# Optimization experiments

Hardware: AMD Instinct MI355X
Metric: run time of the kernel (lower is better)

The kernel has to match this reference:

```python
import jax, jax.numpy as jnp
import numpy as np

K = 3
PAD = 1
STRIDE = 1


def _conv2d(x, w, b, stride, pad):
    y = jax.lax.conv_general_dilated(
        x, w, window_strides=(stride, stride), padding=[(pad, pad), (pad, pad)],
        dimension_numbers=("NCHW", "OIHW", "NCHW"))
    return y + b[None, :, None, None]


def _deform_conv(x, offsets, w_def, stride, pad):
    B, C, H, W = x.shape
    Cout = w_def.shape[0]
    Ho, Wo = offsets.shape[2], offsets.shape[3]
    K2 = K * K
    # torchvision layout: offsets[:, 2*k] = dy, offsets[:, 2*k+1] = dx for tap k = i*K + j
    off = offsets.reshape(B, K2, 2, Ho, Wo)
    dy, dx = off[:, :, 0], off[:, :, 1]  # [B,K2,Ho,Wo]
    k = jnp.arange(K2)
    iy = (k // K).astype(x.dtype)  # kernel tap row
    ix = (k % K).astype(x.dtype)
    hs = (jnp.arange(Ho) * stride - pad).astype(x.dtype)
    ws = (jnp.arange(Wo) * stride - pad).astype(x.dtype)
    py = hs[None, None, :, None] + iy[None, :, None, None] + dy  # [B,K2,Ho,Wo]
    px = ws[None, None, None, :] + ix[None, :, None, None] + dx
    y0 = jnp.floor(py)
    x0 = jnp.floor(px)
    wy = py - y0
    wx = px - x0
    x_flat = x.reshape(B, C, H * W)

    def gather(yi, xi, wgt):
        valid = (yi >= 0) & (yi < H) & (xi >= 0) & (xi < W)
        yic = jnp.clip(yi, 0, H - 1).astype(jnp.int32)
        xic = jnp.clip(xi, 0, W - 1).astype(jnp.int32)
        idx = (yic * W + xic).reshape(B, -1)  # [B, K2*Ho*Wo]
        g = jax.vmap(lambda xf, i: xf[:, i])(x_flat, idx)  # [B,C,K2*Ho*Wo]
        return g * (wgt * valid).reshape(B, 1, -1)

    val = gather(y0, x0, (1 - wy) * (1 - wx))
    val = val + gather(y0, x0 + 1, (1 - wy) * wx)
    val = val + gather(y0 + 1, x0, wy * (1 - wx))
    val = val + gather(y0 + 1, x0 + 1, wy * wx)
    val = val.reshape(B, C, K2, Ho, Wo)  # bilinear-sampled im2col
    return jnp.einsum('bckhw,ock->bohw', val, w_def.reshape(Cout, C, K2))


def setup_inputs() -> dict:
    key = jax.random.key(0)
    k1, k2, k3, k4 = jax.random.split(key, 4)
    B, C, H, W, Cout = 8, 128, 64, 64, 128
    x = jax.random.normal(k1, (B, C, H, W), dtype=jnp.float32)
    w_off = jax.random.normal(k2, (2 * K * K, C, K, K), dtype=jnp.float32) * 0.01
    b_off = jax.random.normal(k3, (2 * K * K,), dtype=jnp.float32) * 0.01
    w_def = jax.random.normal(k4, (Cout, C, K, K), dtype=jnp.float32) * (1.0 / np.sqrt(C * K * K))
    return {"x": x, "w_off": w_off, "b_off": b_off, "w_def": w_def}


def reference(x, w_off, b_off, w_def):
    offsets = _conv2d(x, w_off, b_off, STRIDE, PAD)
    return _deform_conv(x, offsets, w_def, STRIDE, PAD)
```

## Files before the change

### kernel.cpp

```cpp
#include <hip/hip_runtime.h>
#include <hip/hip_bf16.h>

#define B_    8
#define C_    128
#define H_    64
#define W_    64
#define COUT_ 128
#define K2_   9
#define JOFF_ 18
#define HW_   (H_*W_)
#define CK_   (C_*K2_)

typedef short  short8 __attribute__((ext_vector_type(8)));
typedef float  f32x4  __attribute__((ext_vector_type(4)));

__device__ __forceinline__ ushort f2bf(float f) {
    __hip_bfloat16 h = __float2bfloat16(f);
    return *reinterpret_cast<ushort*>(&h);
}
__device__ __forceinline__ float bf2f(ushort u) {
    return __uint_as_float(((uint)u) << 16);
}
__device__ __forceinline__ uint bfround(float f) {
    uint u = __float_as_uint(f);
    return u + 0x7FFFu + ((u >> 16) & 1u);
}
__device__ __forceinline__ uint bfpack(float v0, float v1) {
    return __builtin_amdgcn_perm(bfround(v1), bfround(v0), 0x07060302u);
}

__global__ __launch_bounds__(512) void nhwc_kernel(
    const float* __restrict__ x, ushort* __restrict__ xt)
{
    __shared__ float tile[64][65];
    const int blk = blockIdx.x;
    const int ht = blk & 63;
    const int ct = (blk >> 6) & 1;
    const int b  = blk >> 7;
    const int t  = threadIdx.x;
    const int tx = t & 63, ty = t >> 6;

    const float* xs = x + ((size_t)(b * C_ + ct * 64) << 12) + (ht << 6);
#pragma unroll
    for (int i = 0; i < 8; ++i) {
        int c = i * 8 + ty;
        tile[c][tx] = xs[((size_t)c << 12) + tx];
    }
    __syncthreads();

    const int r  = t >> 3;
    const int co = (t & 7) * 8;
    short8 pack;
#pragma unroll
    for (int j = 0; j < 8; ++j) pack[j] = (short)f2bf(tile[co + j][r]);
    *reinterpret_cast<short8*>(
        xt + ((((size_t)b << 12) + (ht << 6) + r) << 7) + ct * 64 + co) = pack;
}

__global__ __launch_bounds__(256) void transpose_w_kernel(
    const float* __restrict__ w_def, const float* __restrict__ w_off,
    ushort* __restrict__ wt, ushort* __restrict__ wt_off)
{
    int t = blockIdx.x * 256 + threadIdx.x;
    if (t < K2_ * COUT_ * C_) {
        int c = t & 127;
        int o = (t >> 7) & 127;
        int k = t >> 14;
        float v = w_def[((size_t)o * C_ + c) * K2_ + k];
        wt[((size_t)k * COUT_ + o) * C_ + c] = f2bf(v);
    } else {
        int i = t - K2_ * COUT_ * C_;
        if (i < K2_ * 32 * C_) {
            int c = i & 127;
            int j = (i >> 7) & 31;
            int k = i >> 12;
            float v = (j < JOFF_) ? w_off[((size_t)j * C_ + c) * K2_ + k] : 0.f;
            wt_off[(((size_t)k * 32) + j) * C_ + c] = f2bf(v);
        }
    }
}

__global__ __launch_bounds__(512, 4) void deform_mfma_kernel(
    const ushort* __restrict__ xt, const ushort* __restrict__ wt,
    const ushort* __restrict__ wt_off, const float* __restrict__ b_off,
    float* __restrict__ out)
{
    __shared__ __align__(16) ushort smem[3 * 66 * C_];
    __shared__ float s_off[JOFF_][64];

    typedef ushort sB_t[2][64][C_];
    typedef ushort pro_t[3][66][C_];
    sB_t&  sB  = *reinterpret_cast<sB_t*>(smem);
    pro_t& pro = *reinterpret_cast<pro_t*>(smem);

    const int bid  = blockIdx.x;
    const int nbid = ((bid & 7) << 6) + (bid >> 3);
    const int s0   = nbid << 6;
    const int b    = s0 >> 12;
    const int hw0  = s0 & (HW_ - 1);
    const int ho   = hw0 >> 6;

    const int t    = threadIdx.x;
    const int wid  = t >> 6, lane = t & 63;
    const int arow = lane & 15;
    const int akk  = (lane >> 4) << 3;
    const int gp   = t >> 3;
    const int gq   = t & 7;
    const int swzp = (gp & 15) << 3;
    const ushort* xtb = xt + ((size_t)b << 19);

    if (t < 384) {
        int rr  = t >> 7, sub = t & 127;
        int q   = (sub & 64) ? 65 : 0;
        reinterpret_cast<uint*>(&pro[rr][q][0])[sub & 63] = 0u;
    }
#pragma unroll
    for (int it = 0; it < 6; ++it) {
        int i   = t + it * 512;
        int rr  = i >> 10;
        int rem = i & 1023;
        int pos = rem >> 4;
        int ch  = rem & 15;
        int yr  = ho - 1 + rr;
        short8 val = {};
        if (yr >= 0 && yr < H_)
            val = *reinterpret_cast<const short8*>(
                xtb + (((size_t)((yr << 6) + pos)) << 7) + ch * 8);
        int q = pos + 1;
        *reinterpret_cast<short8*>(
            &pro[rr][q][(ch * 8) ^ ((q & 7) << 3)]) = val;
    }
    __syncthreads();

    {
        const int wmO = wid >> 2, wnO = wid & 3;
        const int colq = wnO * 16 + arow;
        f32x4 o0 = {}, o1 = {};
#pragma unroll
        for (int k = 0; k < K2_; ++k) {
            const int ky = k / 3, kx = k % 3;
            const int qr  = colq + kx;
            const int key = (qr & 7) << 3;
            const ushort* ap = wt_off
                + (((size_t)(k * 32 + wmO * 16 + arow)) << 7) + akk;
#pragma unroll
            for (int kc = 0; kc < 4; ++kc) {
                short8 aO = *reinterpret_cast<const short8*>(ap + kc * 32);
                short8 bO = *reinterpret_cast<const short8*>(
                    &pro[ky][qr][(kc * 32 + akk) ^ key]);
                if (kc < 2) o0 = __builtin_amdgcn_mfma_f32_16x16x32_bf16(aO, bO, o0, 0, 0, 0);
                else        o1 = __builtin_amdgcn_mfma_f32_16x16x32_bf16(aO, bO, o1, 0, 0, 0);
            }
        }
        const int sO = wnO * 16 + arow;
#pragma unroll
        for (int r4 = 0; r4 < 4; ++r4) {
            int j = wmO * 16 + ((lane >> 4) << 2) + r4;
            if (j < JOFF_) s_off[j][sO] = o0[r4] + o1[r4] + b_off[j];
        }
    }
    __syncthreads();

    f32x4  acc[4] = {};
    short8 aA[4], aB[4];
    short8 gA[4][2], gB[4][2];
    float  cA[4], cB[4];

    auto load_a = [&](int k, short8 (&dst)[4]) {
        const ushort* wk = wt + (size_t)k * (COUT_ * C_)
                         + (wid * 16 + arow) * C_ + akk;
#pragma unroll
        for (int kc = 0; kc < 4; ++kc)
            dst[kc] = *reinterpret_cast<const short8*>(wk + kc * 32);
    };

    auto gather_load = [&](int k, short8 (&g)[4][2], float (&ca)[4]) {
        float dy = s_off[2*k    ][gp];
        float dx = s_off[2*k + 1][gp];
        float py = (float)(ho - 1 + k/3) + dy;
        float px = (float)(gp - 1 + k%3) + dx;
        float y0f = floorf(py), x0f = floorf(px);
        float wy = py - y0f,    wx = px - x0f;
        int y0 = (int)y0f, x0 = (int)x0f;
        int y1 = y0 + 1,   x1 = x0 + 1;
        float vy0 = (y0 >= 0 && y0 < H_) ? 1.f : 0.f;
        float vy1 = (y1 >= 0 && y1 < H_) ? 1.f : 0.f;
        float vx0 = (x0 >= 0 && x0 < W_) ? 1.f : 0.f;
        float vx1 = (x1 >= 0 && x1 < W_) ? 1.f : 0.f;
        int y0c = min(max(y0, 0), H_-1), y1c = min(max(y1, 0), H_-1);
        int x0c = min(max(x0, 0), W_-1), x1c = min(max(x1, 0), W_-1);
        int bx  = min(max(x0, 0), W_-2);
        float wx0 = (1.f - wx) * vx0, wx1 = wx * vx1;
        float ex0 = (x0c == bx ? wx0 : 0.f) + (x1c == bx ? wx1 : 0.f);
        float ex1 = (x0c == bx ? 0.f : wx0) + (x1c == bx ? 0.f : wx1);
        float r0 = (1.f - wy) * vy0, r1 = wy * vy1;
        ca[0] = r0*ex0; ca[1] = r0*ex1; ca[2] = r1*ex0; ca[3] = r1*ex1;
        const ushort* r00 = xtb + (((y0c << 6) + bx) << 7) + gq * 8;
        const ushort* r10 = xtb + (((y1c << 6) + bx) << 7) + gq * 8;
        g[0][0] = *reinterpret_cast<const short8*>(r00);
        g[0][1] = *reinterpret_cast<const short8*>(r00 + 64);
        g[1][0] = *reinterpret_cast<const short8*>(r00 + 128);
        g[1][1] = *reinterpret_cast<const short8*>(r00 + 192);
        g[2][0] = *reinterpret_cast<const short8*>(r10);
        g[2][1] = *reinterpret_cast<const short8*>(r10 + 64);
        g[3][0] = *reinterpret_cast<const short8*>(r10 + 128);
        g[3][1] = *reinterpret_cast<const short8*>(r10 + 192);
    };

    auto gather_math_store = [&](int buf, const short8 (&g)[4][2],
                                 const float (&ca)[4]) {
#pragma unroll
        for (int j = 0; j < 2; ++j) {
            float v[8];
#pragma unroll
            for (int q = 0; q < 8; ++q) {
                float vv = ca[0] * bf2f((ushort)g[0][j][q]);
                vv = fmaf(ca[1], bf2f((ushort)g[1][j][q]), vv);
                vv = fmaf(ca[2], bf2f((ushort)g[2][j][q]), vv);
                vv = fmaf(ca[3], bf2f((ushort)g[3][j][q]), vv);
                v[q] = vv;
            }
            uint4 pk;
            pk.x = bfpack(v[0], v[1]);
            pk.y = bfpack(v[2], v[3]);
            pk.z = bfpack(v[4], v[5]);
            pk.w = bfpack(v[6], v[7]);
            *reinterpret_cast<uint4*>(
                &sB[buf][gp][(gq * 8 + j * 64) ^ swzp]) = pk;
        }
    };

    load_a(0, aA);
    gather_load(0, gA, cA);
    gather_load(1, gB, cB);
    gather_math_store(0, gA, cA);
    asm volatile("s_waitcnt lgkmcnt(0)" ::: "memory");
    __builtin_amdgcn_s_barrier();

#pragma unroll
    for (int k = 0; k < K2_; ++k) {
        if (k < K2_ - 1) {
            if ((k & 1) == 0) load_a(k + 1, aB);
            else              load_a(k + 1, aA);
        }
        if (k + 2 < K2_) {
            if ((k & 1) == 0) gather_load(k + 2, gA, cA);
            else              gather_load(k + 2, gB, cB);
        }

        {
            const short8 (&a)[4] = ((k & 1) == 0) ? aA : aB;
            const int buf = k & 1;
#pragma unroll
            for (int kc = 0; kc < 4; ++kc) {
#pragma unroll
                for (int ni = 0; ni < 4; ++ni) {
                    int srow = ni*16 + arow;
                    short8 bF = *reinterpret_cast<const short8*>(
                        &sB[buf][srow][(kc*32 + akk) ^ ((srow & 15) << 3)]);
                    acc[ni] = __builtin_amdgcn_mfma_f32_16x16x32_bf16(
                        a[kc], bF, acc[ni], 0, 0, 0);
                }
            }
        }

        if (k < K2_ - 1) {
            if ((k & 1) == 0) gather_math_store((k + 1) & 1, gB, cB);
            else              gather_math_store((k + 1) & 1, gA, cA);
        }

        asm volatile("s_waitcnt lgkmcnt(0)" ::: "memory");
        __builtin_amdgcn_s_barrier();
    }

#pragma unroll
    for (int ni = 0; ni < 4; ++ni) {
#pragma unroll
        for (int r = 0; r < 4; ++r) {
            int o = wid*16 + ((lane >> 4) << 2) + r;
            int s = ni*16 + arow;
            __builtin_nontemporal_store(acc[ni][r],
                &out[(((size_t)(b*COUT_ + o)) << 12) + hw0 + s]);
        }
    }
}

extern "C" void kernel_launch(void* const* d_in, const int* in_sizes, int n_in,
                              void* d_out, int out_size, void* d_ws, size_t ws_size,
                              hipStream_t stream) {
    const float* x     = (const float*)d_in[0];
    const float* w_off = (const float*)d_in[1];
    const float* b_off = (const float*)d_in[2];
    const float* w_def = (const float*)d_in[3];
    float* out  = (float*)d_out;

    char* ws = (char*)d_ws;
    ushort* xtp    = (ushort*)ws;
    ushort* wt     = (ushort*)(ws + 8388608);
    ushort* wt_off = (ushort*)(ws + 8388608 + 294912);

    nhwc_kernel<<<1024, 512, 0, stream>>>(x, xtp);
    {
        int total  = K2_ * COUT_ * C_ + K2_ * 32 * C_;
        transpose_w_kernel<<<(total + 255) / 256, 256, 0, stream>>>(
            w_def, w_off, wt, wt_off);
    }
    deform_mfma_kernel<<<(B_ * HW_) / 64, 512, 0, stream>>>(
        xtp, wt, wt_off, b_off, out);
}
```

Measured before the change: 59.48 us.

## Halve spatial tile to 32 pixels per block and raise occupancy

Each block now covers 32 output pixels instead of 64, which doubles the grid and shrinks the shared-memory prologue and sampling buffers. Launch bounds go from 4 to 6 blocks per CU. The A-weight double buffer becomes a single buffer that is reloaded after the MFMA loop behind a sched_barrier. This lowers register and LDS pressure to gain occupancy, at the cost of reloading the full weight matrix per block and extra halo loads. In the offset conv, waves with wid>=4 now duplicate the work of waves 0-3 and write the same s_off entries.

```diff
diff --git a/kernel.cpp b/kernel.cpp
--- a/kernel.cpp
+++ b/kernel.cpp
@@ -80,60 +80,58 @@
     }
 }
 
-__global__ __launch_bounds__(512, 4) void deform_mfma_kernel(
+__global__ __launch_bounds__(512, 6) void deform_mfma_kernel(
     const ushort* __restrict__ xt, const ushort* __restrict__ wt,
     const ushort* __restrict__ wt_off, const float* __restrict__ b_off,
     float* __restrict__ out)
 {
-    __shared__ __align__(16) ushort smem[3 * 66 * C_];
-    __shared__ float s_off[JOFF_][64];
-
-    typedef ushort sB_t[2][64][C_];
-    typedef ushort pro_t[3][66][C_];
+    __shared__ __align__(16) ushort smem[3 * 34 * C_];
+    __shared__ float s_off[JOFF_][32];
+
+    typedef ushort sB_t[2][32][C_];
+    typedef ushort pro_t[3][34][C_];
     sB_t&  sB  = *reinterpret_cast<sB_t*>(smem);
     pro_t& pro = *reinterpret_cast<pro_t*>(smem);
 
     const int bid  = blockIdx.x;
-    const int nbid = ((bid & 7) << 6) + (bid >> 3);
-    const int s0   = nbid << 6;
+    const int nbid = ((bid & 7) << 7) + (bid >> 3);
+    const int s0   = nbid << 5;
     const int b    = s0 >> 12;
     const int hw0  = s0 & (HW_ - 1);
     const int ho   = hw0 >> 6;
+    const int wo0  = hw0 & 63;
 
     const int t    = threadIdx.x;
     const int wid  = t >> 6, lane = t & 63;
     const int arow = lane & 15;
     const int akk  = (lane >> 4) << 3;
-    const int gp   = t >> 3;
-    const int gq   = t & 7;
+    const int gp   = t >> 4;
+    const int gq   = t & 15;
     const int swzp = (gp & 15) << 3;
     const ushort* xtb = xt + ((size_t)b << 19);
 
-    if (t < 384) {
-        int rr  = t >> 7, sub = t & 127;
-        int q   = (sub & 64) ? 65 : 0;
-        reinterpret_cast<uint*>(&pro[rr][q][0])[sub & 63] = 0u;
-    }
-#pragma unroll
-    for (int it = 0; it < 6; ++it) {
-        int i   = t + it * 512;
-        int rr  = i >> 10;
-        int rem = i & 1023;
-        int pos = rem >> 4;
-        int ch  = rem & 15;
-        int yr  = ho - 1 + rr;
-        short8 val = {};
-        if (yr >= 0 && yr < H_)
-            val = *reinterpret_cast<const short8*>(
-                xtb + (((size_t)((yr << 6) + pos)) << 7) + ch * 8);
-        int q = pos + 1;
-        *reinterpret_cast<short8*>(
-            &pro[rr][q][(ch * 8) ^ ((q & 7) << 3)]) = val;
+#pragma unroll
+    for (int it = 0; it < 4; ++it) {
+        int i = t + it * 512;
+        if (i < 3 * 34 * 16) {
+            int rr  = i / 544;
+            int rem = i - rr * 544;
+            int q   = rem >> 4;
+            int ch  = rem & 15;
+            int yr  = ho - 1 + rr;
+            int sx  = wo0 - 1 + q;
+            short8 val = {};
+            if (yr >= 0 && yr < H_ && sx >= 0 && sx < W_)
+                val = *reinterpret_cast<const short8*>(
+                    xtb + (((size_t)((yr << 6) + sx)) << 7) + ch * 8);
+            *reinterpret_cast<short8*>(
+                &pro[rr][q][(ch * 8) ^ ((q & 7) << 3)]) = val;
+        }
     }
     __syncthreads();
 
     {
-        const int wmO = wid >> 2, wnO = wid & 3;
+        const int wmO = (wid >> 1) & 1, wnO = wid & 1;
         const int colq = wnO * 16 + arow;
         f32x4 o0 = {}, o1 = {};
 #pragma unroll
@@ -161,24 +159,24 @@
     }
     __syncthreads();
 
-    f32x4  acc[4] = {};
-    short8 aA[4], aB[4];
-    short8 gA[4][2], gB[4][2];
+    f32x4  acc[2] = {};
+    short8 aC[4];
+    short8 gA[4], gB[4];
     float  cA[4], cB[4];
 
-    auto load_a = [&](int k, short8 (&dst)[4]) {
+    auto load_a = [&](int k) {
         const ushort* wk = wt + (size_t)k * (COUT_ * C_)
                          + (wid * 16 + arow) * C_ + akk;
 #pragma unroll
         for (int kc = 0; kc < 4; ++kc)
-            dst[kc] = *reinterpret_cast<const short8*>(wk + kc * 32);
+            aC[kc] = *reinterpret_cast<const short8*>(wk + kc * 32);
     };
 
-    auto gather_load = [&](int k, short8 (&g)[4][2], float (&ca)[4]) {
+    auto gather_load = [&](int k, short8 (&g)[4], float (&ca)[4]) {
         float dy = s_off[2*k    ][gp];
         float dx = s_off[2*k + 1][gp];
         float py = (float)(ho - 1 + k/3) + dy;
-        float px = (float)(gp - 1 + k%3) + dx;
+        float px = (float)(wo0 + gp - 1 + k%3) + dx;
         float y0f = floorf(py), x0f = floorf(px);
         float wy = py - y0f,    wx = px - x0f;
         int y0 = (int)y0f, x0 = (int)x0f;
@@ -197,40 +195,32 @@
         ca[0] = r0*ex0; ca[1] = r0*ex1; ca[2] = r1*ex0; ca[3] = r1*ex1;
         const ushort* r00 = xtb + (((y0c << 6) + bx) << 7) + gq * 8;
         const ushort* r10 = xtb + (((y1c << 6) + bx) << 7) + gq * 8;
-        g[0][0] = *reinterpret_cast<const short8*>(r00);
-        g[0][1] = *reinterpret_cast<const short8*>(r00 + 64);
-        g[1][0] = *reinterpret_cast<const short8*>(r00 + 128);
-        g[1][1] = *reinterpret_cast<const short8*>(r00 + 192);
-        g[2][0] = *reinterpret_cast<const short8*>(r10);
-        g[2][1] = *reinterpret_cast<const short8*>(r10 + 64);
-        g[3][0] = *reinterpret_cast<const short8*>(r10 + 128);
-        g[3][1] = *reinterpret_cast<const short8*>(r10 + 192);
+        g[0] = *reinterpret_cast<const short8*>(r00);
+        g[1] = *reinterpret_cast<const short8*>(r00 + 128);
+        g[2] = *reinterpret_cast<const short8*>(r10);
+        g[3] = *reinterpret_cast<const short8*>(r10 + 128);
     };
 
-    auto gather_math_store = [&](int buf, const short8 (&g)[4][2],
+    auto gather_math_store = [&](int buf, const short8 (&g)[4],
                                  const float (&ca)[4]) {
-#pragma unroll
-        for (int j = 0; j < 2; ++j) {
-            float v[8];
-#pragma unroll
-            for (int q = 0; q < 8; ++q) {
-                float vv = ca[0] * bf2f((ushort)g[0][j][q]);
-                vv = fmaf(ca[1], bf2f((ushort)g[1][j][q]), vv);
-                vv = fmaf(ca[2], bf2f((ushort)g[2][j][q]), vv);
-                vv = fmaf(ca[3], bf2f((ushort)g[3][j][q]), vv);
-                v[q] = vv;
-            }
-            uint4 pk;
-            pk.x = bfpack(v[0], v[1]);
-            pk.y = bfpack(v[2], v[3]);
-            pk.z = bfpack(v[4], v[5]);
-            pk.w = bfpack(v[6], v[7]);
-            *reinterpret_cast<uint4*>(
-                &sB[buf][gp][(gq * 8 + j * 64) ^ swzp]) = pk;
-        }
+        float v[8];
+#pragma unroll
+        for (int q = 0; q < 8; ++q) {
+            float vv = ca[0] * bf2f((ushort)g[0][q]);
+            vv = fmaf(ca[1], bf2f((ushort)g[1][q]), vv);
+            vv = fmaf(ca[2], bf2f((ushort)g[2][q]), vv);
+            vv = fmaf(ca[3], bf2f((ushort)g[3][q]), vv);
+            v[q] = vv;
+        }
+        uint4 pk;
+        pk.x = bfpack(v[0], v[1]);
+        pk.y = bfpack(v[2], v[3]);
+        pk.z = bfpack(v[4], v[5]);
+        pk.w = bfpack(v[6], v[7]);
+        *reinterpret_cast<uint4*>(&sB[buf][gp][(gq * 8) ^ swzp]) = pk;
     };
 
-    load_a(0, aA);
+    load_a(0);
     gather_load(0, gA, cA);
     gather_load(1, gB, cB);
     gather_math_store(0, gA, cA);
@@ -239,32 +229,30 @@
 
 #pragma unroll
     for (int k = 0; k < K2_; ++k) {
-        if (k < K2_ - 1) {
-            if ((k & 1) == 0) load_a(k + 1, aB);
-            else              load_a(k + 1, aA);
-        }
         if (k + 2 < K2_) {
             if ((k & 1) == 0) gather_load(k + 2, gA, cA);
             else              gather_load(k + 2, gB, cB);
         }
 
         {
-            const short8 (&a)[4] = ((k & 1) == 0) ? aA : aB;
             const int buf = k & 1;
 #pragma unroll
             for (int kc = 0; kc < 4; ++kc) {
 #pragma unroll
-                for (int ni = 0; ni < 4; ++ni) {
+                for (int ni = 0; ni < 2; ++ni) {
                     int srow = ni*16 + arow;
                     short8 bF = *reinterpret_cast<const short8*>(
                         &sB[buf][srow][(kc*32 + akk) ^ ((srow & 15) << 3)]);
                     acc[ni] = __builtin_amdgcn_mfma_f32_16x16x32_bf16(
-                        a[kc], bF, acc[ni], 0, 0, 0);
+                        aC[kc], bF, acc[ni], 0, 0, 0);
                 }
             }
         }
 
+        __builtin_amdgcn_sched_barrier(0);
+
         if (k < K2_ - 1) {
+            load_a(k + 1);
             if ((k & 1) == 0) gather_math_store((k + 1) & 1, gB, cB);
             else              gather_math_store((k + 1) & 1, gA, cA);
         }
@@ -274,7 +262,7 @@
     }
 
 #pragma unroll
-    for (int ni = 0; ni < 4; ++ni) {
+    for (int ni = 0; ni < 2; ++ni) {
 #pragma unroll
         for (int r = 0; r < 4; ++r) {
             int o = wid*16 + ((lane >> 4) << 2) + r;
@@ -305,6 +293,6 @@
         transpose_w_kernel<<<(total + 255) / 256, 256, 0, stream>>>(
             w_def, w_off, wt, wt_off);
     }
-    deform_mfma_kernel<<<(B_ * HW_) / 64, 512, 0, stream>>>(
+    deform_mfma_kernel<<<(B_ * HW_) / 32, 512, 0, stream>>>(
         xtp, wt, wt_off, b_off, out);
 }
```

After: 103.9 us. 1.75x slower.

## Merge prep kernels and retile deform GEMM warps to 2x2 fragments

Applied to the files above, without the earlier changes.

Fuses the NHWC transpose and weight transpose kernels into one prep launch to save a kernel launch. In the main kernel, each wave now computes a 32x32 output tile (2x2 MFMA fragments) instead of a 16x64 strip. This reuses each B fragment read from LDS for two MFMAs, halving LDS reads of the sampled im2col. The A-weight load moves after the MFMA block behind a sched_barrier and is no longer double-buffered, which may expose global-load latency.

```diff
diff --git a/kernel.cpp b/kernel.cpp
--- a/kernel.cpp
+++ b/kernel.cpp
@@ -29,51 +29,49 @@
     return __builtin_amdgcn_perm(bfround(v1), bfround(v0), 0x07060302u);
 }
 
-__global__ __launch_bounds__(512) void nhwc_kernel(
-    const float* __restrict__ x, ushort* __restrict__ xt)
-{
-    __shared__ float tile[64][65];
-    const int blk = blockIdx.x;
-    const int ht = blk & 63;
-    const int ct = (blk >> 6) & 1;
-    const int b  = blk >> 7;
-    const int t  = threadIdx.x;
-    const int tx = t & 63, ty = t >> 6;
-
-    const float* xs = x + ((size_t)(b * C_ + ct * 64) << 12) + (ht << 6);
-#pragma unroll
-    for (int i = 0; i < 8; ++i) {
-        int c = i * 8 + ty;
-        tile[c][tx] = xs[((size_t)c << 12) + tx];
-    }
-    __syncthreads();
-
-    const int r  = t >> 3;
-    const int co = (t & 7) * 8;
-    short8 pack;
-#pragma unroll
-    for (int j = 0; j < 8; ++j) pack[j] = (short)f2bf(tile[co + j][r]);
-    *reinterpret_cast<short8*>(
-        xt + ((((size_t)b << 12) + (ht << 6) + r) << 7) + ct * 64 + co) = pack;
-}
-
-__global__ __launch_bounds__(256) void transpose_w_kernel(
-    const float* __restrict__ w_def, const float* __restrict__ w_off,
+__global__ __launch_bounds__(512) void prep_kernel(
+    const float* __restrict__ x, const float* __restrict__ w_def,
+    const float* __restrict__ w_off, ushort* __restrict__ xt,
     ushort* __restrict__ wt, ushort* __restrict__ wt_off)
 {
-    int t = blockIdx.x * 256 + threadIdx.x;
-    if (t < K2_ * COUT_ * C_) {
-        int c = t & 127;
-        int o = (t >> 7) & 127;
-        int k = t >> 14;
-        float v = w_def[((size_t)o * C_ + c) * K2_ + k];
-        wt[((size_t)k * COUT_ + o) * C_ + c] = f2bf(v);
+    const int blk = blockIdx.x;
+    const int t   = threadIdx.x;
+
+    if (blk < 1024) {
+        __shared__ float tile[64][65];
+        const int ht = blk & 63;
+        const int ct = (blk >> 6) & 1;
+        const int b  = blk >> 7;
+        const int tx = t & 63, ty = t >> 6;
+
+        const float* xs = x + ((size_t)(b * C_ + ct * 64) << 12) + (ht << 6);
+#pragma unroll
+        for (int i = 0; i < 8; ++i) {
+            int c = i * 8 + ty;
+            tile[c][tx] = xs[((size_t)c << 12) + tx];
+        }
+        __syncthreads();
+
+        const int r  = t >> 3;
+        const int co = (t & 7) * 8;
+        short8 pack;
+#pragma unroll
+        for (int j = 0; j < 8; ++j) pack[j] = (short)f2bf(tile[co + j][r]);
+        *reinterpret_cast<short8*>(
+            xt + ((((size_t)b << 12) + (ht << 6) + r) << 7) + ct * 64 + co) = pack;
     } else {
-        int i = t - K2_ * COUT_ * C_;
-        if (i < K2_ * 32 * C_) {
+        int i = (blk - 1024) * 512 + t;
+        if (i < K2_ * COUT_ * C_) {
             int c = i & 127;
-            int j = (i >> 7) & 31;
-            int k = i >> 12;
+            int o = (i >> 7) & 127;
+            int k = i >> 14;
+            float v = w_def[((size_t)o * C_ + c) * K2_ + k];
+            wt[((size_t)k * COUT_ + o) * C_ + c] = f2bf(v);
+        } else {
+            int j2 = i - K2_ * COUT_ * C_;
+            int c = j2 & 127;
+            int j = (j2 >> 7) & 31;
+            int k = j2 >> 12;
             float v = (j < JOFF_) ? w_off[((size_t)j * C_ + c) * K2_ + k] : 0.f;
             wt_off[(((size_t)k * 32) + j) * C_ + c] = f2bf(v);
         }
@@ -161,17 +159,22 @@
     }
     __syncthreads();
 
-    f32x4  acc[4] = {};
-    short8 aA[4], aB[4];
+    const int wmD = wid >> 1;
+    const int wnD = wid & 1;
+
+    f32x4  acc[2][2] = {};
+    short8 aC[2][4];
     short8 gA[4][2], gB[4][2];
     float  cA[4], cB[4];
 
-    auto load_a = [&](int k, short8 (&dst)[4]) {
-        const ushort* wk = wt + (size_t)k * (COUT_ * C_)
-                         + (wid * 16 + arow) * C_ + akk;
-#pragma unroll
-        for (int kc = 0; kc < 4; ++kc)
-            dst[kc] = *reinterpret_cast<const short8*>(wk + kc * 32);
+    auto load_a = [&](int k) {
+        const ushort* wk = wt + (size_t)k * (COUT_ * C_) + akk;
+#pragma unroll
+        for (int mi = 0; mi < 2; ++mi)
+#pragma unroll
+            for (int kc = 0; kc < 4; ++kc)
+                aC[mi][kc] = *reinterpret_cast<const short8*>(
+                    wk + (wmD * 32 + mi * 16 + arow) * C_ + kc * 32);
     };
 
     auto gather_load = [&](int k, short8 (&g)[4][2], float (&ca)[4]) {
@@ -230,7 +233,7 @@
         }
     };
 
-    load_a(0, aA);
+    load_a(0);
     gather_load(0, gA, cA);
     gather_load(1, gB, cB);
     gather_math_store(0, gA, cA);
@@ -239,32 +242,32 @@
 
 #pragma unroll
     for (int k = 0; k < K2_; ++k) {
-        if (k < K2_ - 1) {
-            if ((k & 1) == 0) load_a(k + 1, aB);
-            else              load_a(k + 1, aA);
-        }
         if (k + 2 < K2_) {
             if ((k & 1) == 0) gather_load(k + 2, gA, cA);
             else              gather_load(k + 2, gB, cB);
         }
 
         {
-            const short8 (&a)[4] = ((k & 1) == 0) ? aA : aB;
             const int buf = k & 1;
 #pragma unroll
             for (int kc = 0; kc < 4; ++kc) {
 #pragma unroll
-                for (int ni = 0; ni < 4; ++ni) {
-                    int srow = ni*16 + arow;
+                for (int ni = 0; ni < 2; ++ni) {
+                    int srow = wnD * 32 + ni * 16 + arow;
                     short8 bF = *reinterpret_cast<const short8*>(
                         &sB[buf][srow][(kc*32 + akk) ^ ((srow & 15) << 3)]);
-                    acc[ni] = __builtin_amdgcn_mfma_f32_16x16x32_bf16(
-                        a[kc], bF, acc[ni], 0, 0, 0);
+#pragma unroll
+                    for (int mi = 0; mi < 2; ++mi)
+                        acc[mi][ni] = __builtin_amdgcn_mfma_f32_16x16x32_bf16(
+                            aC[mi][kc], bF, acc[mi][ni], 0, 0, 0);
                 }
             }
         }
 
+        __builtin_amdgcn_sched_barrier(0);
+
         if (k < K2_ - 1) {
+            load_a(k + 1);
             if ((k & 1) == 0) gather_math_store((k + 1) & 1, gB, cB);
             else              gather_math_store((k + 1) & 1, gA, cA);
         }
@@ -274,13 +277,16 @@
     }
 
 #pragma unroll
-    for (int ni = 0; ni < 4; ++ni) {
-#pragma unroll
-        for (int r = 0; r < 4; ++r) {
-            int o = wid*16 + ((lane >> 4) << 2) + r;
-            int s = ni*16 + arow;
-            __builtin_nontemporal_store(acc[ni][r],
-                &out[(((size_t)(b*COUT_ + o)) << 12) + hw0 + s]);
+    for (int mi = 0; mi < 2; ++mi) {
+#pragma unroll
+        for (int ni = 0; ni < 2; ++ni) {
+#pragma unroll
+            for (int r = 0; r < 4; ++r) {
+                int o = wmD*32 + mi*16 + ((lane >> 4) << 2) + r;
+                int s = wnD*32 + ni*16 + arow;
+                __builtin_nontemporal_store(acc[mi][ni][r],
+                    &out[(((size_t)(b*COUT_ + o)) << 12) + hw0 + s]);
+            }
         }
     }
 }
@@ -299,12 +305,7 @@
     ushort* wt     = (ushort*)(ws + 8388608);
     ushort* wt_off = (ushort*)(ws + 8388608 + 294912);
 
-    nhwc_kernel<<<1024, 512, 0, stream>>>(x, xtp);
-    {
-        int total  = K2_ * COUT_ * C_ + K2_ * 32 * C_;
-        transpose_w_kernel<<<(total + 255) / 256, 256, 0, stream>>>(
-            w_def, w_off, wt, wt_off);
-    }
+    prep_kernel<<<1384, 512, 0, stream>>>(x, w_def, w_off, xtp, wt, wt_off);
     deform_mfma_kernel<<<(B_ * HW_) / 64, 512, 0, stream>>>(
         xtp, wt, wt_off, b_off, out);
 }
```

Measured after the change: 89.84 us. +51.1%, slower.
